# Kernel optimization log

Measured on AMD Instinct MI355X. Metric: run time of the kernel, lower is better.

## Reference

```python
import jax, jax.numpy as jnp
import numpy as np


def setup_inputs() -> dict:
    key = jax.random.key(0)
    ks = jax.random.split(key, 7)
    batch, hidden, k = 16384, 1024, 16
    return {
        "A": jax.random.normal(ks[0], (batch, hidden), dtype=jnp.float32),
        "B": jax.random.normal(ks[1], (batch, hidden), dtype=jnp.float32),
        "W": jax.random.normal(ks[2], (k, hidden, hidden), dtype=jnp.float32),
        "V_w": jax.random.normal(ks[3], (k, 2 * hidden), dtype=jnp.float32) * 0.02,
        "V_b": jax.random.normal(ks[4], (k,), dtype=jnp.float32) * 0.02,
        "out_w": jax.random.normal(ks[5], (1, k), dtype=jnp.float32) * 0.02,
        "out_b": jax.random.normal(ks[6], (1,), dtype=jnp.float32) * 0.02,
    }


def reference(A, B, W, V_w, V_b, out_b, out_w):
    # Bilinear tensor scores: score[b,i] = sum_d (A @ W[i])[b,d] * B[b,d]
    # Batched over k instead of the original python loop.
    AW = jnp.einsum("bh,khd->bkd", A, W)          # [batch, k, hidden]
    tensor_scores = jnp.einsum("bkd,bd->bk", AW, B)  # [batch, k]
    # Linear fusion on concatenated pair features.
    linear = jnp.concatenate([A, B], axis=1) @ V_w.T + V_b  # [batch, k]
    h = jnp.tanh(tensor_scores + linear)
    return (h @ out_w.T + out_b).squeeze(-1)  # [batch]
```

## Files before the change

### kernel.cpp

```cpp
#include <hip/hip_runtime.h>
#include <hip/hip_bf16.h>
#include <stdint.h>

typedef __bf16 bf16x8 __attribute__((ext_vector_type(8)));
typedef float  f32x4  __attribute__((ext_vector_type(4)));
typedef unsigned short ushort_t;

#define BATCH 16384
#define HID   1024
#define KK    16
#define NKB   32
#define BM    256
#define BN    256
#define BUFS  32768
#define LDSW_OFF 16384

__device__ __forceinline__ unsigned short bf16_rne(float x) {
    uint32_t u = __float_as_uint(x);
    uint32_t r = (u + 0x7fffu + ((u >> 16) & 1u)) >> 16;
    return (unsigned short)r;
}
__device__ __forceinline__ void split2(float x, unsigned short& h, unsigned short& l) {
    h = bf16_rne(x);
    float hf = __uint_as_float(((uint32_t)h) << 16);
    l = bf16_rne(x - hf);
}

__global__ __launch_bounds__(256) void k_split_a(const float* __restrict__ A,
                                                 ushort_t* __restrict__ Acomb) {
    uint32_t q   = blockIdx.x * 256u + threadIdx.x;
    uint32_t b   = q >> 7;
    uint32_t rem = q & 127u;
    uint32_t kb  = rem >> 2;
    uint32_t cq  = rem & 3u;
    const float* src = A + (size_t)b * HID + kb * 32 + cq * 8;
    float4 v0 = *(const float4*)src;
    float4 v1 = *(const float4*)(src + 4);
    ushort_t h[8], l[8];
    split2(v0.x, h[0], l[0]); split2(v0.y, h[1], l[1]);
    split2(v0.z, h[2], l[2]); split2(v0.w, h[3], l[3]);
    split2(v1.x, h[4], l[4]); split2(v1.y, h[5], l[5]);
    split2(v1.z, h[6], l[6]); split2(v1.w, h[7], l[7]);
    ushort_t* row = Acomb + ((size_t)kb * BATCH + b) * 64;
    uint32_t sw = b & 7u;
    *(uint4*)(row + ((cq      ) ^ sw) * 8) = *(uint4*)h;
    *(uint4*)(row + ((cq + 4u) ^ sw) * 8) = *(uint4*)l;
}

__global__ __launch_bounds__(256) void k_split_w(const float* __restrict__ W,
                                                 ushort_t* __restrict__ Wcomb) {
    int bx = blockIdx.x;
    int i  = bx >> 9;
    int kb = (bx >> 4) & 31;
    int dt = bx & 15;
    __shared__ float lds[32][65];
    const float* src = W + ((size_t)i * HID + (size_t)kb * 32) * HID + dt * 64;
    int t = threadIdx.x;
    #pragma unroll
    for (int rep = 0; rep < 8; ++rep) {
        int lin = rep * 256 + t;
        int hl = lin >> 6, dl = lin & 63;
        lds[hl][dl] = src[(size_t)hl * HID + dl];
    }
    __syncthreads();
    #pragma unroll
    for (int rep = 0; rep < 2; ++rep) {
        int cid = rep * 256 + t;
        int dl = cid >> 3, qq = cid & 7;
        ushort_t outv[8];
        #pragma unroll
        for (int j = 0; j < 8; ++j) {
            int col = qq * 8 + j;
            float x = (col < 32) ? lds[col][dl] : lds[col - 32][dl];
            unsigned short h, l; split2(x, h, l);
            outv[j] = (col < 32) ? h : l;
        }
        *(uint4*)(Wcomb + ((((size_t)i * NKB + kb) * HID) + dt * 64 + dl) * 64
                  + (qq ^ (dl & 7)) * 8) = *(uint4*)outv;
    }
}

#define BAR() asm volatile("s_barrier" ::: "memory")
#define GLL(gsrc, dstIdx) \
    __builtin_amdgcn_global_load_lds((const __attribute__((address_space(1))) void*)(gsrc), \
        (__attribute__((address_space(3))) void*)(&smem[(dstIdx)]), 16, 0, 0)

__global__ __launch_bounds__(512, 2) void k_gemm(const ushort_t* __restrict__ Acomb,
                                                 const ushort_t* __restrict__ Wcomb,
                                                 const float* __restrict__ B,
                                                 float* __restrict__ score) {
    __shared__ __align__(16) ushort_t smem[2 * BUFS];
    const int tid  = threadIdx.x;
    const int lane = tid & 63;
    const int wave = tid >> 6;
    const int wm = wave >> 2, wn = wave & 3;
    const int l15 = lane & 15, l4 = lane >> 4;
    const int brow = blockIdx.x * BM;
    const int dcol = blockIdx.y * BN;
    const int i    = blockIdx.z;

    f32x4 acc[8][4];
    #pragma unroll
    for (int m = 0; m < 8; ++m)
        #pragma unroll
        for (int n = 0; n < 4; ++n)
            acc[m][n] = (f32x4){0.f, 0.f, 0.f, 0.f};

    const int csw_hi = ((l4    ) ^ (l15 & 7)) * 8;
    const int csw_lo = ((l4 + 4) ^ (l15 & 7)) * 8;
    const int aoff_hi = (wm * 128 + l15) * 64 + csw_hi;
    const int aoff_lo = (wm * 128 + l15) * 64 + csw_lo;
    const int woff_hi = LDSW_OFF + (wn * 64 + l15) * 64 + csw_hi;
    const int woff_lo = LDSW_OFF + (wn * 64 + l15) * 64 + csw_lo;

    const ushort_t* gA0 = Acomb + ((size_t)brow + wave * 16) * 64 + lane * 8;
    const ushort_t* gW0 = Wcomb + ((size_t)i * NKB * HID + dcol + wave * 16) * 64 + lane * 8;
    const int sdst = wave * 1024;

#define STAGE_A(c, t1, h) do { \
    const ushort_t* g_ = gA0 + ((size_t)(t1) * BATCH + (h) * 128) * 64; \
    GLL(g_,       (c) * BUFS + (h) * 8192 + sdst); \
    GLL(g_ + 512, (c) * BUFS + (h) * 8192 + sdst + 512); \
  } while (0)
#define STAGE_W(c, t1, h) do { \
    const ushort_t* g_ = gW0 + ((size_t)(t1) * HID + (h) * 128) * 64; \
    GLL(g_,       (c) * BUFS + LDSW_OFF + (h) * 8192 + sdst); \
    GLL(g_ + 512, (c) * BUFS + LDSW_OFF + (h) * 8192 + sdst + 512); \
  } while (0)

    bf16x8 ah[4], al[4], wh[4], wl[4];
#define RD_W(n, cb) do { \
    wh[n] = *(const bf16x8*)(&smem[(cb) + woff_hi + (n) * 1024]); \
    wl[n] = *(const bf16x8*)(&smem[(cb) + woff_lo + (n) * 1024]); } while (0)
#define RD_A(m, slot, cb) do { \
    ah[slot] = *(const bf16x8*)(&smem[(cb) + aoff_hi + (m) * 1024]); \
    al[slot] = *(const bf16x8*)(&smem[(cb) + aoff_lo + (m) * 1024]); } while (0)

#define MFMA_Q(MB, NB) do { \
    __builtin_amdgcn_s_setprio(1); \
    _Pragma("unroll") \
    for (int mm = 0; mm < 4; ++mm) { \
      _Pragma("unroll") \
      for (int nn = 0; nn < 2; ++nn) \
        acc[(MB)+mm][(NB)+nn] = __builtin_amdgcn_mfma_f32_16x16x32_bf16(ah[mm], wh[(NB)+nn], acc[(MB)+mm][(NB)+nn], 0, 0, 0); } \
    _Pragma("unroll") \
    for (int mm = 0; mm < 4; ++mm) { \
      _Pragma("unroll") \
      for (int nn = 0; nn < 2; ++nn) \
        acc[(MB)+mm][(NB)+nn] = __builtin_amdgcn_mfma_f32_16x16x32_bf16(ah[mm], wl[(NB)+nn], acc[(MB)+mm][(NB)+nn], 0, 0, 0); } \
    _Pragma("unroll") \
    for (int mm = 0; mm < 4; ++mm) { \
      _Pragma("unroll") \
      for (int nn = 0; nn < 2; ++nn) \
        acc[(MB)+mm][(NB)+nn] = __builtin_amdgcn_mfma_f32_16x16x32_bf16(al[mm], wh[(NB)+nn], acc[(MB)+mm][(NB)+nn], 0, 0, 0); } \
    __builtin_amdgcn_s_setprio(0); \
  } while (0)

#define TILE_BODY(c, t, DOSTAGE) do { \
    const int cb = (c) * BUFS; \
     \
    if (DOSTAGE) { STAGE_A((c) ^ 1, (t) + 1, 0); STAGE_A((c) ^ 1, (t) + 1, 1); } \
    RD_W(0, cb); RD_W(1, cb); \
    RD_A(0, 0, cb); RD_A(1, 1, cb); RD_A(2, 2, cb); RD_A(3, 3, cb); \
    BAR(); \
    MFMA_Q(0, 0); \
    BAR(); \
     \
    if (DOSTAGE) { STAGE_W((c) ^ 1, (t) + 1, 0); STAGE_W((c) ^ 1, (t) + 1, 1); } \
    RD_W(2, cb); RD_W(3, cb); \
    BAR(); \
    MFMA_Q(0, 2); \
    BAR(); \
     \
    RD_A(4, 0, cb); RD_A(5, 1, cb); RD_A(6, 2, cb); RD_A(7, 3, cb); \
    BAR(); \
    MFMA_Q(4, 0); \
    BAR(); \
     \
    MFMA_Q(4, 2); \
    __syncthreads(); \
  } while (0)

    STAGE_A(0, 0, 0); STAGE_A(0, 0, 1);
    STAGE_W(0, 0, 0); STAGE_W(0, 0, 1);
    __syncthreads();

    int cur = 0;
    for (int t = 0; t < NKB - 1; ++t) {
        TILE_BODY(cur, t, 1);
        cur ^= 1;
    }
    TILE_BODY(cur, NKB - 1, 0);

    #pragma unroll
    for (int m = 0; m < 8; ++m) {
        #pragma unroll
        for (int r = 0; r < 4; ++r) {
            int row = brow + wm * 128 + m * 16 + l4 * 4 + r;
            const float* Brow = B + (size_t)row * HID + dcol + wn * 64 + l15;
            float s = acc[m][0][r] * Brow[0]
                    + acc[m][1][r] * Brow[16]
                    + acc[m][2][r] * Brow[32]
                    + acc[m][3][r] * Brow[48];
            s += __shfl_xor(s, 1);
            s += __shfl_xor(s, 2);
            s += __shfl_xor(s, 4);
            s += __shfl_xor(s, 8);
            if (l15 == 0) atomicAdd(&score[(size_t)row * KK + i], s);
        }
    }
}

__global__ __launch_bounds__(256) void k_linear(const float* __restrict__ A,
                                                const float* __restrict__ B,
                                                const float* __restrict__ Vw,
                                                const float* __restrict__ Vb,
                                                float* __restrict__ lin) {
    __shared__ float4 sA[128][9];
    __shared__ float4 sB[128][9];
    __shared__ float4 sVa[16][9];
    __shared__ float4 sVb[16][9];
    const int t = threadIdx.x;
    const int brow = blockIdx.x * 128;
    const int b_loc = t >> 1;
    const int ihalf = t & 1;
    float acc8[8] = {0.f, 0.f, 0.f, 0.f, 0.f, 0.f, 0.f, 0.f};

    for (int hc = 0; hc < HID; hc += 32) {
        __syncthreads();
        #pragma unroll
        for (int rep = 0; rep < 4; ++rep) {
            int idx = rep * 256 + t;
            int bl = idx >> 3, h4 = idx & 7;
            sA[bl][h4] = *(const float4*)(A + (size_t)(brow + bl) * HID + hc + h4 * 4);
            sB[bl][h4] = *(const float4*)(B + (size_t)(brow + bl) * HID + hc + h4 * 4);
        }
        if (t < 128) {
            int ii = t >> 3, h4 = t & 7;
            sVa[ii][h4] = *(const float4*)(Vw + (size_t)ii * 2048 + hc + h4 * 4);
        } else {
            int tt = t - 128;
            int ii = tt >> 3, h4 = tt & 7;
            sVb[ii][h4] = *(const float4*)(Vw + (size_t)ii * 2048 + 1024 + hc + h4 * 4);
        }
        __syncthreads();
        #pragma unroll
        for (int h4 = 0; h4 < 8; ++h4) {
            float4 a4 = sA[b_loc][h4];
            float4 b4 = sB[b_loc][h4];
            #pragma unroll
            for (int ii = 0; ii < 8; ++ii) {
                int iG = ihalf * 8 + ii;
                float4 va = sVa[iG][h4], vb = sVb[iG][h4];
                acc8[ii] += a4.x * va.x + a4.y * va.y + a4.z * va.z + a4.w * va.w
                          + b4.x * vb.x + b4.y * vb.y + b4.z * vb.z + b4.w * vb.w;
            }
        }
    }
    #pragma unroll
    for (int ii = 0; ii < 8; ++ii) {
        int iG = ihalf * 8 + ii;
        lin[(size_t)(brow + b_loc) * KK + iG] = acc8[ii] + Vb[iG];
    }
}

__global__ __launch_bounds__(256) void k_final(const float* __restrict__ score,
                                               const float* __restrict__ lin,
                                               const float* __restrict__ out_w,
                                               const float* __restrict__ out_b,
                                               float* __restrict__ out) {
    int b = blockIdx.x * 256 + threadIdx.x;
    float o = out_b[0];
    #pragma unroll
    for (int i = 0; i < KK; ++i)
        o += out_w[i] * tanhf(score[(size_t)b * KK + i] + lin[(size_t)b * KK + i]);
    out[b] = o;
}

extern "C" void kernel_launch(void* const* d_in, const int* in_sizes, int n_in,
                              void* d_out, int out_size, void* d_ws, size_t ws_size,
                              hipStream_t stream) {
    (void)in_sizes; (void)n_in; (void)out_size; (void)ws_size;
    const float* A     = (const float*)d_in[0];
    const float* B     = (const float*)d_in[1];
    const float* W     = (const float*)d_in[2];
    const float* Vw    = (const float*)d_in[3];
    const float* Vb    = (const float*)d_in[4];
    const float* out_w = (const float*)d_in[5];
    const float* out_b = (const float*)d_in[6];
    float* out = (float*)d_out;

    ushort_t* Acomb = (ushort_t*)d_ws;
    ushort_t* Wcomb = Acomb + (size_t)NKB * BATCH * 64;
    float* score = (float*)(Wcomb + (size_t)KK * NKB * HID * 64);
    float* lin   = score + (size_t)BATCH * KK;

    hipMemsetAsync(score, 0, (size_t)BATCH * KK * sizeof(float), stream);
    k_split_a<<<dim3(8192), dim3(256), 0, stream>>>(A, Acomb);
    k_split_w<<<dim3(8192), dim3(256), 0, stream>>>(W, Wcomb);
    k_gemm<<<dim3(BATCH / BM, HID / BN, KK), dim3(512), 0, stream>>>(Acomb, Wcomb, B, score);
    k_linear<<<dim3(BATCH / 128), dim3(256), 0, stream>>>(A, B, Vw, Vb, lin);
    k_final<<<dim3(BATCH / 256), dim3(256), 0, stream>>>(score, lin, out_w, out_b, out);
}
```

Measured before the change: 1.647 ms.

## Prefetch two tiles ahead with vmcnt-gated barriers instead of per-quarter barriers

Restructures the K-loop so each LDS buffer is refilled right after its compute finishes. Two tiles are kept in flight, and the wait before using a buffer is a counted s_waitcnt vmcnt(8) rather than a full drain. It also removes the intra-tile s_barriers between MFMA quarters, leaving only two barriers per tile boundary, so waves can drift and the per-tile synchronization cost drops. The risks are a longer stall at the boundary and LDS reads contending with async global-to-LDS writes. Correctness also depends on the vmcnt counting matching the eight loads issued per tile.

```diff
diff --git a/kernel.cpp b/kernel.cpp
--- a/kernel.cpp
+++ b/kernel.cpp
@@ -80,7 +80,6 @@
     }
 }
 
-#define BAR() asm volatile("s_barrier" ::: "memory")
 #define GLL(gsrc, dstIdx) \
     __builtin_amdgcn_global_load_lds((const __attribute__((address_space(1))) void*)(gsrc), \
         (__attribute__((address_space(3))) void*)(&smem[(dstIdx)]), 16, 0, 0)
@@ -126,6 +125,10 @@
     const ushort_t* g_ = gW0 + ((size_t)(t1) * HID + (h) * 128) * 64; \
     GLL(g_,       (c) * BUFS + LDSW_OFF + (h) * 8192 + sdst); \
     GLL(g_ + 512, (c) * BUFS + LDSW_OFF + (h) * 8192 + sdst + 512); \
+  } while (0)
+#define STAGE_TILE(c, t1) do { \
+    STAGE_A(c, t1, 0); STAGE_A(c, t1, 1); \
+    STAGE_W(c, t1, 0); STAGE_W(c, t1, 1); \
   } while (0)
 
     bf16x8 ah[4], al[4], wh[4], wl[4];
@@ -156,41 +159,44 @@
     __builtin_amdgcn_s_setprio(0); \
   } while (0)
 
-#define TILE_BODY(c, t, DOSTAGE) do { \
-    const int cb = (c) * BUFS; \
-     \
-    if (DOSTAGE) { STAGE_A((c) ^ 1, (t) + 1, 0); STAGE_A((c) ^ 1, (t) + 1, 1); } \
+#define TILE_COMPUTE(cb) do { \
     RD_W(0, cb); RD_W(1, cb); \
     RD_A(0, 0, cb); RD_A(1, 1, cb); RD_A(2, 2, cb); RD_A(3, 3, cb); \
-    BAR(); \
     MFMA_Q(0, 0); \
-    BAR(); \
-     \
-    if (DOSTAGE) { STAGE_W((c) ^ 1, (t) + 1, 0); STAGE_W((c) ^ 1, (t) + 1, 1); } \
     RD_W(2, cb); RD_W(3, cb); \
-    BAR(); \
     MFMA_Q(0, 2); \
-    BAR(); \
-     \
     RD_A(4, 0, cb); RD_A(5, 1, cb); RD_A(6, 2, cb); RD_A(7, 3, cb); \
-    BAR(); \
     MFMA_Q(4, 0); \
-    BAR(); \
-     \
     MFMA_Q(4, 2); \
-    __syncthreads(); \
-  } while (0)
-
-    STAGE_A(0, 0, 0); STAGE_A(0, 0, 1);
-    STAGE_W(0, 0, 0); STAGE_W(0, 0, 1);
-    __syncthreads();
-
-    int cur = 0;
-    for (int t = 0; t < NKB - 1; ++t) {
-        TILE_BODY(cur, t, 1);
-        cur ^= 1;
-    }
-    TILE_BODY(cur, NKB - 1, 0);
+  } while (0)
+
+#define TILE_BOUNDARY(c, t2) do { \
+    asm volatile("s_waitcnt lgkmcnt(0)" ::: "memory"); \
+    __builtin_amdgcn_s_barrier(); \
+    __builtin_amdgcn_sched_barrier(0); \
+    if ((t2) < NKB) { \
+        STAGE_TILE(c, t2); \
+        asm volatile("s_waitcnt vmcnt(8)" ::: "memory"); \
+    } else { \
+        asm volatile("s_waitcnt vmcnt(0)" ::: "memory"); \
+    } \
+    __builtin_amdgcn_s_barrier(); \
+    __builtin_amdgcn_sched_barrier(0); \
+  } while (0)
+
+    STAGE_TILE(0, 0);
+    STAGE_TILE(1, 1);
+    asm volatile("s_waitcnt vmcnt(8)" ::: "memory");
+    __builtin_amdgcn_s_barrier();
+    __builtin_amdgcn_sched_barrier(0);
+
+    #pragma unroll 1
+    for (int t = 0; t < NKB; t += 2) {
+        TILE_COMPUTE(0);
+        TILE_BOUNDARY(0, t + 2);
+        TILE_COMPUTE(BUFS);
+        TILE_BOUNDARY(1, t + 3);
+    }
 
     #pragma unroll
     for (int m = 0; m < 8; ++m) {
```

After: 1.718 ms. 1.04x slower.
